# Optimization experiments

Hardware: AMD Instinct MI355X
Metric: run time of the kernel (lower is better)

## Reference

```python
import jax, jax.numpy as jnp
import numpy as np

NUM_HEADS = 12


def setup_inputs() -> dict:
    key = jax.random.key(0)
    k1, k2, k3 = jax.random.split(key, 3)
    B, N, D = 8, 1024, 768
    x = jax.random.normal(k1, (B, N, D), dtype=jnp.float32)
    Wqkv = jax.random.normal(k2, (D, 3 * D), dtype=jnp.float32) * (D ** -0.5)
    Wproj = jax.random.normal(k3, (D, D), dtype=jnp.float32) * (D ** -0.5)
    bproj = jnp.zeros((D,), dtype=jnp.float32)
    return {"x": x, "Wqkv": Wqkv, "Wproj": Wproj, "bproj": bproj}


def reference(x, Wqkv, Wproj, bproj):
    B, N, D = x.shape
    H = NUM_HEADS
    d = D // H
    scale = d ** -0.5
    qkv = x @ Wqkv  # [B, N, 3D]; qkv_bias=False
    # 'b n (qkv h d) -> qkv b h n d'
    qkv = qkv.reshape(B, N, 3, H, d)
    q = jnp.transpose(qkv[:, :, 0], (0, 2, 1, 3))  # [B, H, N, d]
    k = jnp.transpose(qkv[:, :, 1], (0, 2, 1, 3))
    v = jnp.transpose(qkv[:, :, 2], (0, 2, 1, 3))
    attn = jnp.einsum('bhnd,bhmd->bhnm', q, k) * scale  # [B, H, N, N]
    attn = jax.nn.softmax(attn, axis=-1)
    out = jnp.einsum('bhnm,bhmd->bhnd', attn, v)  # [B, H, N, d]
    out = jnp.transpose(out, (0, 2, 1, 3)).reshape(B, N, D)  # 'b h n d -> b n (h d)'
    return out @ Wproj + bproj
```

## Files before the change

kernel.cpp:

```cpp
#include <hip/hip_runtime.h>
#include <math.h>
#include <stdint.h>

namespace {

constexpr int Nseq = 1024;
constexpr int Dm = 768;
constexpr int threeD = 2304;
constexpr int Mrows = 8192;
constexpr int Hh = 12;
constexpr float kScaleLog2 = 0.18033688011112042f;

using bf16x8 = __attribute__((ext_vector_type(8))) short;
using f32x4 = __attribute__((ext_vector_type(4))) float;
using f32x16 = __attribute__((ext_vector_type(16))) float;
using us4 = __attribute__((ext_vector_type(4))) unsigned short;

__device__ __forceinline__ unsigned short f2bf(float f) {
  union { float f; uint32_t u; } v;
  v.f = f;
  uint32_t r = v.u + 0x7fffu + ((v.u >> 16) & 1u);
  return (unsigned short)(r >> 16);
}

__device__ __forceinline__ float fexp2(float x) {
#if __has_builtin(__builtin_amdgcn_exp2f)
  return __builtin_amdgcn_exp2f(x);
#else
  float r;
  asm("v_exp_f32 %0, %1\n\ts_nop 0" : "=v"(r) : "v"(x));
  return r;
#endif
}

__device__ __forceinline__ uint32_t cvtpk_bf16(float lo, float hi) {
  uint32_t r;
  asm("v_cvt_pk_bf16_f32 %0, %1, %2" : "=v"(r) : "v"(lo), "v"(hi));
  return r;
}

__device__ __forceinline__ void gload_lds16(const void* g, void* l) {
  __builtin_amdgcn_global_load_lds(
      (const __attribute__((address_space(1))) unsigned int*)(uintptr_t)g,
      (__attribute__((address_space(3))) unsigned int*)(uintptr_t)l, 16, 0, 0);
}

__global__ __launch_bounds__(256) void prep_all(
    const float* __restrict__ x, const float* __restrict__ Wqkv,
    const float* __restrict__ Wproj, unsigned short* __restrict__ xb,
    unsigned short* __restrict__ wqkvt, unsigned short* __restrict__ wprojt) {
  __shared__ unsigned short tile[32][33];
  const int bid = blockIdx.x;
  if (bid < 6144) {
    const int i = bid * 256 + threadIdx.x;
    float4 v = ((const float4*)x)[i];
    us4 u = {f2bf(v.x), f2bf(v.y), f2bf(v.z), f2bf(v.w)};
    ((us4*)xb)[i] = u;
    return;
  }
  const float* W;
  unsigned short* Wt;
  int N, t;
  if (bid < 6144 + 1728) {
    W = Wqkv;
    Wt = wqkvt;
    N = threeD;
    t = bid - 6144;
  } else {
    W = Wproj;
    Wt = wprojt;
    N = Dm;
    t = bid - 6144 - 1728;
  }
  const int nx = N / 32;
  const int n0 = (t % nx) * 32, k0 = (t / nx) * 32;
  const int tx = threadIdx.x & 31, ty = threadIdx.x >> 5;
#pragma unroll
  for (int i = 0; i < 32; i += 8)
    tile[ty + i][tx] = f2bf(W[(size_t)(k0 + ty + i) * N + n0 + tx]);
  __syncthreads();
#pragma unroll
  for (int i = 0; i < 32; i += 8)
    Wt[(size_t)(n0 + ty + i) * 768 + k0 + tx] = tile[tx][ty + i];
}

template <int MODE, int BM, int NCOLS>
__global__ __launch_bounds__(256) void gemm_bf16(
    const unsigned short* __restrict__ A, const unsigned short* __restrict__ Bt,
    void* __restrict__ C0, void* __restrict__ C1,
    const float* __restrict__ bias, int K) {
  constexpr int ASL = BM * 4;
  constexpr int TS = ASL + 512;
  constexpr int LPS = TS / 256;
  constexpr int MF = BM / 32;
  __shared__ unsigned short As[3][ASL * 8];
  __shared__ unsigned short Bs[3][512 * 8];
  const int tid = threadIdx.x;
  const int wid = tid >> 6;
  const int lane = tid & 63;
  const int l15 = lane & 15, lg = lane >> 4;
  const int p = blockIdx.x;
  const int cpx = gridDim.x >> 3;
  const int l = (p & 7) * cpx + (p >> 3);
  const int row0 = (l / NCOLS) * BM, col0 = (l % NCOLS) * 128;
  const int wr = (wid >> 1) * (BM / 2), wc = (wid & 1) * 64;

  auto stage = [&](int k0, int bufi) {
    unsigned short* as = As[bufi];
    unsigned short* bs = Bs[bufi];
#pragma unroll
    for (int it = 0; it < LPS; ++it) {
      const int s = it * 256 + tid;
      if (s < ASL) {
        const int r = s >> 2, c = s & 3;
        const int g = c ^ ((r >> 1) & 3);
        gload_lds16(&A[(size_t)(row0 + r) * K + k0 + g * 8],
                    &as[(s & ~63) * 8]);
      } else {
        const int s2 = s - ASL;
        const int r = s2 >> 2, c = s2 & 3;
        const int g = c ^ ((r >> 1) & 3);
        gload_lds16(&Bt[(size_t)(col0 + r) * K + k0 + g * 8],
                    &bs[(s2 & ~63) * 8]);
      }
    }
  };

  f32x4 acc[MF][4] = {};
  const int nt = K / 32;
  stage(0, 0);
  stage(32, 1);
  for (int t = 0; t < nt; ++t) {
    const int cur = t % 3;
    if (t + 2 < nt) {
      stage((t + 2) * 32, (t + 2) % 3);
      asm volatile("s_waitcnt vmcnt(%0)" ::"i"(2 * LPS) : "memory");
    } else if (t + 1 < nt) {
      asm volatile("s_waitcnt vmcnt(%0)" ::"i"(LPS) : "memory");
    } else {
      asm volatile("s_waitcnt vmcnt(0)" ::: "memory");
    }
    __builtin_amdgcn_s_barrier();
    bf16x8 av[MF], bv[4];
#pragma unroll
    for (int m = 0; m < MF; ++m) {
      const int ar = wr + m * 16 + l15;
      av[m] = *(const bf16x8*)&As[cur][(ar * 4 + (lg ^ ((ar >> 1) & 3))) * 8];
    }
#pragma unroll
    for (int n = 0; n < 4; ++n) {
      const int br = wc + n * 16 + l15;
      bv[n] = *(const bf16x8*)&Bs[cur][(br * 4 + (lg ^ ((br >> 1) & 3))) * 8];
    }
#pragma unroll
    for (int m = 0; m < MF; ++m)
#pragma unroll
      for (int n = 0; n < 4; ++n)
        acc[m][n] =
            __builtin_amdgcn_mfma_f32_16x16x32_bf16(av[m], bv[n], acc[m][n], 0, 0, 0);
    asm volatile("s_waitcnt lgkmcnt(0)" ::: "memory");
    __builtin_amdgcn_sched_barrier(0);
    __builtin_amdgcn_s_barrier();
  }
  if constexpr (MODE == 1) {
#pragma unroll
    for (int m = 0; m < MF; ++m)
#pragma unroll
      for (int n = 0; n < 4; ++n) {
        const int col = col0 + wc + n * 16 + l15;
#pragma unroll
        for (int rr = 0; rr < 4; ++rr)
          ((float*)C0)[(size_t)(row0 + wr + m * 16 + lg * 4 + rr) * Dm + col] =
              acc[m][n][rr] + bias[col];
      }
  } else if (col0 < 1536) {
#pragma unroll
    for (int m = 0; m < MF; ++m)
#pragma unroll
      for (int n = 0; n < 4; ++n) {
        const int col = col0 + wc + n * 16 + l15;
        const float qs = (col < 768) ? kScaleLog2 : 1.f;
#pragma unroll
        for (int rr = 0; rr < 4; ++rr)
          ((unsigned short*)C0)[(size_t)(row0 + wr + m * 16 + lg * 4 + rr) * 1536 +
                                col] = f2bf(acc[m][n][rr] * qs);
      }
  } else {
#pragma unroll
    for (int m = 0; m < MF; ++m)
#pragma unroll
      for (int n = 0; n < 4; ++n) {
        const int c = col0 + wc + n * 16 + l15 - 1536;
        const int row = row0 + wr + m * 16 + lg * 4;
        const int bb = row >> 10, n0 = row & 1023;
        us4 pk = {f2bf(acc[m][n][0]), f2bf(acc[m][n][1]), f2bf(acc[m][n][2]),
                  f2bf(acc[m][n][3])};
        *(us4*)&((unsigned short*)C1)[((size_t)bb * 768 + c) * 1024 + n0] = pk;
      }
  }
}

__global__ __launch_bounds__(256) void attn_mfma(
    const unsigned short* __restrict__ qkb, const unsigned short* __restrict__ vtb,
    unsigned short* __restrict__ outb) {
  constexpr int NT = Nseq / 64;
  __shared__ unsigned short Ks[3][64 * 64];
  __shared__ unsigned short Vs[3][64 * 64];
  const int tid = threadIdx.x;
  const int wid = tid >> 6, lane = tid & 63;
  const int l31 = lane & 31, hi = lane >> 5;
  const int p = blockIdx.x;
  const int l = (p & 7) * 96 + (p >> 3);
  const int qt = l & 7;
  const int hb = l >> 3;
  const int h = hb % Hh, b = hb / Hh;
  const size_t rb = (size_t)b * Nseq;
  const int hoff = h * 64;
  const size_t vbase = ((size_t)b * 768 + hoff) * 1024;

  const int qrow = qt * 128 + wid * 32 + l31;
  bf16x8 Qf[4];
#pragma unroll
  for (int ks = 0; ks < 4; ++ks)
    Qf[ks] = *(const bf16x8*)&qkb[(rb + qrow) * 1536 + hoff + ks * 16 + hi * 8];

  int strow[2], scol[2];
#pragma unroll
  for (int it = 0; it < 2; ++it) {
    const int ci = it * 256 + wid * 64 + lane;
    const int tr = ci >> 3, cc = ci & 7;
    strow[it] = tr;
    scol[it] = (cc ^ (tr & 7)) * 8;
  }

  auto stage = [&](int kt, int bufi) {
#pragma unroll
    for (int it = 0; it < 2; ++it) {
      const int ldsoff = (it * 256 + wid * 64) * 8;
      gload_lds16(&qkb[(rb + kt * 64 + strow[it]) * 1536 + 768 + hoff + scol[it]],
                  &Ks[bufi][ldsoff]);
      gload_lds16(&vtb[vbase + (size_t)strow[it] * 1024 + kt * 64 + scol[it]],
                  &Vs[bufi][ldsoff]);
    }
  };

  float l_run = 0.f;
  f32x16 o0 = {}, o1 = {};

  auto qk = [&](int bidx, f32x16& d0, f32x16& d1) {
    const unsigned short* ksb = Ks[bidx];
    d0 = {};
    d1 = {};
    __builtin_amdgcn_s_setprio(1);
#pragma unroll
    for (int ks = 0; ks < 4; ++ks) {
      const int c = 2 * ks + hi;
      {
        const int tr = l31;
        bf16x8 kf = *(const bf16x8*)&ksb[tr * 64 + ((c ^ (tr & 7)) * 8)];
        d0 = __builtin_amdgcn_mfma_f32_32x32x16_bf16(kf, Qf[ks], d0, 0, 0, 0);
      }
      {
        const int tr = l31 + 32;
        bf16x8 kf = *(const bf16x8*)&ksb[tr * 64 + ((c ^ (tr & 7)) * 8)];
        d1 = __builtin_amdgcn_mfma_f32_32x32x16_bf16(kf, Qf[ks], d1, 0, 0, 0);
      }
    }
    __builtin_amdgcn_s_setprio(0);
  };

  auto finish = [&](int bidx, f32x16& s0, f32x16& s1) {
#pragma unroll
    for (int i = 0; i < 16; ++i) {
      s0[i] = fexp2(s0[i]);
      s1[i] = fexp2(s1[i]);
    }
    float a[8];
#pragma unroll
    for (int i = 0; i < 8; ++i)
      a[i] = (s0[i] + s0[i + 8]) + (s1[i] + s1[i + 8]);
#pragma unroll
    for (int st = 4; st >= 1; st >>= 1)
#pragma unroll
      for (int i = 0; i < st; ++i) a[i] += a[i + st];
    l_run += a[0];
    bf16x8 Pf[4];
#pragma unroll
    for (int ks = 0; ks < 4; ++ks) {
      const f32x16 sv = (ks >> 1) ? s1 : s0;
      const int e0 = 8 * (ks & 1);
      uint32_t pe01 = cvtpk_bf16(sv[e0 + 0], sv[e0 + 1]);
      uint32_t pe23 = cvtpk_bf16(sv[e0 + 2], sv[e0 + 3]);
      uint32_t po01 = cvtpk_bf16(sv[e0 + 4], sv[e0 + 5]);
      uint32_t po23 = cvtpk_bf16(sv[e0 + 6], sv[e0 + 7]);
      asm("v_permlane32_swap_b32 %0, %1" : "+v"(pe01), "+v"(po01));
      asm("v_permlane32_swap_b32 %0, %1" : "+v"(pe23), "+v"(po23));
      union {
        uint32_t w[4];
        bf16x8 v;
      } u;
      u.w[0] = pe01;
      u.w[1] = pe23;
      u.w[2] = po01;
      u.w[3] = po23;
      Pf[ks] = u.v;
    }
    const unsigned short* vsb = Vs[bidx];
    __builtin_amdgcn_s_setprio(1);
#pragma unroll
    for (int ks = 0; ks < 4; ++ks) {
      const int c = 2 * ks + hi;
      {
        const int tr = l31;
        bf16x8 vf = *(const bf16x8*)&vsb[tr * 64 + ((c ^ (tr & 7)) * 8)];
        o0 = __builtin_amdgcn_mfma_f32_32x32x16_bf16(vf, Pf[ks], o0, 0, 0, 0);
      }
      {
        const int tr = l31 + 32;
        bf16x8 vf = *(const bf16x8*)&vsb[tr * 64 + ((c ^ (tr & 7)) * 8)];
        o1 = __builtin_amdgcn_mfma_f32_32x32x16_bf16(vf, Pf[ks], o1, 0, 0, 0);
      }
    }
    __builtin_amdgcn_s_setprio(0);
  };

  auto step = [&](int t, f32x16& c0, f32x16& c1, f32x16& n0, f32x16& n1) {
    if (t + 2 < NT) {
      stage(t + 2, (t + 2) % 3);
      asm volatile("s_waitcnt vmcnt(4)" ::: "memory");
    } else {
      asm volatile("s_waitcnt vmcnt(0)" ::: "memory");
    }
    __builtin_amdgcn_s_barrier();
    if (t + 1 < NT) qk((t + 1) % 3, n0, n1);
    finish(t % 3, c0, c1);
    asm volatile("s_waitcnt lgkmcnt(0)" ::: "memory");
    __builtin_amdgcn_sched_barrier(0);
    __builtin_amdgcn_s_barrier();
  };

  stage(0, 0);
  stage(1, 1);
  asm volatile("s_waitcnt vmcnt(4)" ::: "memory");
  __builtin_amdgcn_s_barrier();
  f32x16 sA0, sA1, sB0, sB1;
  qk(0, sA0, sA1);
  for (int t = 0; t < NT; t += 2) {
    step(t, sA0, sA1, sB0, sB1);
    step(t + 1, sB0, sB1, sA0, sA1);
  }
  const float lsum = l_run + __shfl_xor(l_run, 32);
  const float linv = 1.f / lsum;
  const size_t obase = (size_t)(rb + qrow) * Dm + hoff;
#pragma unroll
  for (int g = 0; g < 4; ++g) {
    us4 a4 = {f2bf(o0[g * 4 + 0] * linv), f2bf(o0[g * 4 + 1] * linv),
              f2bf(o0[g * 4 + 2] * linv), f2bf(o0[g * 4 + 3] * linv)};
    *(us4*)&outb[obase + g * 8 + hi * 4] = a4;
    us4 b4 = {f2bf(o1[g * 4 + 0] * linv), f2bf(o1[g * 4 + 1] * linv),
              f2bf(o1[g * 4 + 2] * linv), f2bf(o1[g * 4 + 3] * linv)};
    *(us4*)&outb[obase + 32 + g * 8 + hi * 4] = b4;
  }
}

}

extern "C" void kernel_launch(void* const* d_in, const int* in_sizes, int n_in,
                              void* d_out, int out_size, void* d_ws,
                              size_t ws_size, hipStream_t stream) {
  (void)in_sizes;
  (void)n_in;
  (void)out_size;
  (void)ws_size;
  const float* x = (const float*)d_in[0];
  const float* Wqkv = (const float*)d_in[1];
  const float* Wproj = (const float*)d_in[2];
  const float* bproj = (const float*)d_in[3];
  float* out = (float*)d_out;

  char* w = (char*)d_ws;
  unsigned short* xb = (unsigned short*)w;
  w += (size_t)Mrows * Dm * 2;
  unsigned short* wqkvt = (unsigned short*)w;
  w += (size_t)threeD * Dm * 2;
  unsigned short* wprojt = (unsigned short*)w;
  w += (size_t)Dm * Dm * 2;
  unsigned short* qkb = (unsigned short*)w;
  w += (size_t)Mrows * 1536 * 2;
  unsigned short* vtb = (unsigned short*)w;
  w += (size_t)96 * 64 * 1024 * 2;
  unsigned short* attnb = (unsigned short*)w;

  prep_all<<<dim3(6144 + 1728 + 576), 256, 0, stream>>>(x, Wqkv, Wproj, xb,
                                                        wqkvt, wprojt);
  gemm_bf16<0, 128, 18><<<dim3(1152), 256, 0, stream>>>(
      xb, wqkvt, qkb, vtb, nullptr, Dm);
  attn_mfma<<<dim3(768), 256, 0, stream>>>(qkb, vtb, attnb);
  gemm_bf16<1, 64, 6><<<dim3(768), 256, 0, stream>>>(
      attnb, wprojt, out, nullptr, bproj, Dm);
}
```

Baseline: 116.8 us.

## Use 512-thread attention blocks with 256 queries and double-buffered K/V

The attention kernel now runs 8 waves per block, each block covering 256 query rows instead of 128. Each K/V tile loaded into LDS is therefore shared by twice as many waves, halving global K/V traffic per query. The three-buffer software pipeline, which overlapped the next QK^T with the current softmax/PV, is replaced by a simple double-buffered loop with one stage in flight. Less LDS per block and launch_bounds(512,4) aim at higher occupancy, at the cost of less overlap inside each wave.

```diff
diff --git a/kernel.cpp b/kernel.cpp
--- a/kernel.cpp
+++ b/kernel.cpp
@@ -200,57 +200,57 @@
   }
 }
 
-__global__ __launch_bounds__(256) void attn_mfma(
+__global__ __launch_bounds__(512, 4) void attn_mfma(
     const unsigned short* __restrict__ qkb, const unsigned short* __restrict__ vtb,
     unsigned short* __restrict__ outb) {
   constexpr int NT = Nseq / 64;
-  __shared__ unsigned short Ks[3][64 * 64];
-  __shared__ unsigned short Vs[3][64 * 64];
+  __shared__ unsigned short Ks[2][64 * 64];
+  __shared__ unsigned short Vs[2][64 * 64];
   const int tid = threadIdx.x;
   const int wid = tid >> 6, lane = tid & 63;
   const int l31 = lane & 31, hi = lane >> 5;
   const int p = blockIdx.x;
-  const int l = (p & 7) * 96 + (p >> 3);
-  const int qt = l & 7;
-  const int hb = l >> 3;
+  const int l = (p & 7) * 48 + (p >> 3);
+  const int qt2 = l & 3;
+  const int hb = l >> 2;
   const int h = hb % Hh, b = hb / Hh;
   const size_t rb = (size_t)b * Nseq;
   const int hoff = h * 64;
   const size_t vbase = ((size_t)b * 768 + hoff) * 1024;
 
-  const int qrow = qt * 128 + wid * 32 + l31;
+  const int qrow = qt2 * 256 + wid * 32 + l31;
   bf16x8 Qf[4];
 #pragma unroll
   for (int ks = 0; ks < 4; ++ks)
     Qf[ks] = *(const bf16x8*)&qkb[(rb + qrow) * 1536 + hoff + ks * 16 + hi * 8];
 
-  int strow[2], scol[2];
-#pragma unroll
-  for (int it = 0; it < 2; ++it) {
-    const int ci = it * 256 + wid * 64 + lane;
-    const int tr = ci >> 3, cc = ci & 7;
-    strow[it] = tr;
-    scol[it] = (cc ^ (tr & 7)) * 8;
-  }
+  const int strow = tid >> 3;
+  const int scol = ((tid & 7) ^ (strow & 7)) * 8;
+  const int ldsoff = (wid * 64) * 8;
 
   auto stage = [&](int kt, int bufi) {
-#pragma unroll
-    for (int it = 0; it < 2; ++it) {
-      const int ldsoff = (it * 256 + wid * 64) * 8;
-      gload_lds16(&qkb[(rb + kt * 64 + strow[it]) * 1536 + 768 + hoff + scol[it]],
-                  &Ks[bufi][ldsoff]);
-      gload_lds16(&vtb[vbase + (size_t)strow[it] * 1024 + kt * 64 + scol[it]],
-                  &Vs[bufi][ldsoff]);
-    }
+    gload_lds16(&qkb[(rb + kt * 64 + strow) * 1536 + 768 + hoff + scol],
+                &Ks[bufi][ldsoff]);
+    gload_lds16(&vtb[vbase + (size_t)strow * 1024 + kt * 64 + scol],
+                &Vs[bufi][ldsoff]);
   };
 
   float l_run = 0.f;
   f32x16 o0 = {}, o1 = {};
 
-  auto qk = [&](int bidx, f32x16& d0, f32x16& d1) {
-    const unsigned short* ksb = Ks[bidx];
-    d0 = {};
-    d1 = {};
+  stage(0, 0);
+  for (int kt = 0; kt < NT; ++kt) {
+    const int bufi = kt & 1;
+    if (kt + 1 < NT) {
+      stage(kt + 1, bufi ^ 1);
+      asm volatile("s_waitcnt vmcnt(2)" ::: "memory");
+    } else {
+      asm volatile("s_waitcnt vmcnt(0)" ::: "memory");
+    }
+    __builtin_amdgcn_s_barrier();
+    const unsigned short* ksb = Ks[bufi];
+    const unsigned short* vsb = Vs[bufi];
+    f32x16 s0 = {}, s1 = {};
     __builtin_amdgcn_s_setprio(1);
 #pragma unroll
     for (int ks = 0; ks < 4; ++ks) {
@@ -258,18 +258,15 @@
       {
         const int tr = l31;
         bf16x8 kf = *(const bf16x8*)&ksb[tr * 64 + ((c ^ (tr & 7)) * 8)];
-        d0 = __builtin_amdgcn_mfma_f32_32x32x16_bf16(kf, Qf[ks], d0, 0, 0, 0);
+        s0 = __builtin_amdgcn_mfma_f32_32x32x16_bf16(kf, Qf[ks], s0, 0, 0, 0);
       }
       {
         const int tr = l31 + 32;
         bf16x8 kf = *(const bf16x8*)&ksb[tr * 64 + ((c ^ (tr & 7)) * 8)];
-        d1 = __builtin_amdgcn_mfma_f32_32x32x16_bf16(kf, Qf[ks], d1, 0, 0, 0);
+        s1 = __builtin_amdgcn_mfma_f32_32x32x16_bf16(kf, Qf[ks], s1, 0, 0, 0);
       }
     }
     __builtin_amdgcn_s_setprio(0);
-  };
-
-  auto finish = [&](int bidx, f32x16& s0, f32x16& s1) {
 #pragma unroll
     for (int i = 0; i < 16; ++i) {
       s0[i] = fexp2(s0[i]);
@@ -305,7 +302,6 @@
       u.w[3] = po23;
       Pf[ks] = u.v;
     }
-    const unsigned short* vsb = Vs[bidx];
     __builtin_amdgcn_s_setprio(1);
 #pragma unroll
     for (int ks = 0; ks < 4; ++ks) {
@@ -322,32 +318,9 @@
       }
     }
     __builtin_amdgcn_s_setprio(0);
-  };
-
-  auto step = [&](int t, f32x16& c0, f32x16& c1, f32x16& n0, f32x16& n1) {
-    if (t + 2 < NT) {
-      stage(t + 2, (t + 2) % 3);
-      asm volatile("s_waitcnt vmcnt(4)" ::: "memory");
-    } else {
-      asm volatile("s_waitcnt vmcnt(0)" ::: "memory");
-    }
-    __builtin_amdgcn_s_barrier();
-    if (t + 1 < NT) qk((t + 1) % 3, n0, n1);
-    finish(t % 3, c0, c1);
     asm volatile("s_waitcnt lgkmcnt(0)" ::: "memory");
     __builtin_amdgcn_sched_barrier(0);
     __builtin_amdgcn_s_barrier();
-  };
-
-  stage(0, 0);
-  stage(1, 1);
-  asm volatile("s_waitcnt vmcnt(4)" ::: "memory");
-  __builtin_amdgcn_s_barrier();
-  f32x16 sA0, sA1, sB0, sB1;
-  qk(0, sA0, sA1);
-  for (int t = 0; t < NT; t += 2) {
-    step(t, sA0, sA1, sB0, sB1);
-    step(t + 1, sB0, sB1, sA0, sA1);
   }
   const float lsum = l_run + __shfl_xor(l_run, 32);
   const float linv = 1.f / lsum;
@@ -395,7 +368,7 @@
                                                         wqkvt, wprojt);
   gemm_bf16<0, 128, 18><<<dim3(1152), 256, 0, stream>>>(
       xb, wqkvt, qkb, vtb, nullptr, Dm);
-  attn_mfma<<<dim3(768), 256, 0, stream>>>(qkb, vtb, attnb);
+  attn_mfma<<<dim3(384), 512, 0, stream>>>(qkb, vtb, attnb);
   gemm_bf16<1, 64, 6><<<dim3(768), 256, 0, stream>>>(
       attnb, wprojt, out, nullptr, bproj, Dm);
 }
```

Measured after the change: 116.7 us. About the same (-0.1%).
